# Kernel optimization log

Hardware: AMD Instinct MI355X
Metric: run time of the kernel (lower is better)

Reference implementation:

```python
import jax, jax.numpy as jnp
import numpy as np

NEG_SLOPE = 0.2

def setup_inputs() -> dict:
    key = jax.random.key(0)
    k1, k2, k3, k4 = jax.random.split(key, 4)
    B, n, d_in, d_out = 8, 2048, 128, 128
    x = jax.random.normal(k1, (B, n, d_in), dtype=jnp.float32)
    adj = jax.random.uniform(k2, (B, n, n), dtype=jnp.float32)
    # glorot init for W: std = sqrt(2/(fan_in+fan_out))
    W = jax.random.normal(k3, (d_in, d_out), dtype=jnp.float32) * np.sqrt(2.0 / (d_in + d_out))
    a = jax.random.normal(k4, (2 * d_out,), dtype=jnp.float32) * np.sqrt(2.0 / (2 * d_out + 1))
    return {"x": x, "adj": adj, "W": W, "a": a}

def reference(x, adj, W, a):
    d_out = W.shape[1]
    h = jnp.einsum('bni,io->bno', x, W)               # [B,n,d_out]
    x_weighted = jnp.einsum('bnm,bmo->bno', adj, h)   # adj @ Wx
    # additive attention: a @ concat(h_i, h_j) == h_i@a_src + h_j@a_dst
    a_src, a_dst = a[:d_out], a[d_out:]
    s_i = h @ a_src                                   # [B,n]
    s_j = h @ a_dst                                   # [B,n]
    e = jax.nn.leaky_relu(s_i[:, :, None] + s_j[:, None, :], NEG_SLOPE)  # [B,n,n]
    alpha = jax.nn.softmax(e, axis=2)
    out = jnp.einsum('bnm,bmo->bno', alpha, h) + x_weighted
    return jax.nn.leaky_relu(out, NEG_SLOPE)
```

## Files before the change

kernel.cpp:

```cpp
#include <hip/hip_runtime.h>
#include <hip/hip_bf16.h>

#define NEG 0.2f
#define LOG2E 1.4426950408889634f

typedef __attribute__((ext_vector_type(8))) short bf16x8;
typedef __attribute__((ext_vector_type(4))) float f32x4;
typedef __attribute__((ext_vector_type(16))) float f32x16;
typedef __attribute__((ext_vector_type(4))) int int4v;
typedef __attribute__((ext_vector_type(2))) int int2v;

__device__ __forceinline__ float lrelu(float t){ return fmaxf(t, NEG * t); }
__device__ __forceinline__ float fast_exp2(float x){
  float r; asm("v_exp_f32 %0, %1" : "=v"(r) : "v"(x)); return r;
}
__device__ __forceinline__ unsigned short f2bf(float f){
  union { float f; unsigned int u; } v; v.f = f;
  unsigned int r = v.u + 0x7FFFu + ((v.u >> 16) & 1u);
  return (unsigned short)(r >> 16);
}

__global__ __launch_bounds__(256) void k0_wt(const float* __restrict__ W,
                                             unsigned short* __restrict__ Wt){
  __shared__ __align__(16) unsigned short wl[128*136];
  const int t = threadIdx.x;
  {
    const int k = t >> 1, oh = (t & 1) * 64;
#pragma unroll 8
    for (int e = 0; e < 64; ++e)
      wl[(oh + e)*136 + k] = f2bf(W[k*128 + oh + e]);
  }
  __syncthreads();
  {
    const int o = t >> 1, ks = (t & 1) * 64;
#pragma unroll
    for (int g = 0; g < 8; ++g){
      int4v v = *(const int4v*)(wl + o*136 + ks + g*8);
      *(int4v*)(Wt + o*128 + ks + g*8) = v;
    }
  }
}

__global__ __launch_bounds__(256) void k1_fused(const float* __restrict__ x,
                                                const unsigned short* __restrict__ Wt,
                                                const float* __restrict__ a,
                                                unsigned short* __restrict__ ht,
                                                float* __restrict__ ssrcL,
                                                float* __restrict__ sdstL){
  __shared__ __align__(16) unsigned short wtl[128*136];
  __shared__ __align__(16) unsigned short xl[32*136];
  __shared__ __align__(16) unsigned short tlw[128*34];
  __shared__ float sred[2][4][2][16];
  const int t = threadIdx.x;
  const int bx = blockIdx.x;
  const int b  = bx >> 6;
  const int jt = bx & 63;
  const long rowbase = (long)bx * 32;
  {
    const int o = t >> 1, seg = (t & 1) * 64;
    const int4v* src = (const int4v*)(Wt + o*128 + seg);
    int4v* dst = (int4v*)(wtl + o*136 + seg);
#pragma unroll
    for (int g = 0; g < 8; ++g) dst[g] = src[g];
  }
  {
    const int i = t >> 3, ks = (t & 7) * 16;
    const f32x4* src = (const f32x4*)(x + (rowbase + i)*128 + ks);
    unsigned int q[8];
#pragma unroll
    for (int g = 0; g < 4; ++g){
      f32x4 v = src[g];
      q[g*2]   = (unsigned)f2bf(v[0]) | ((unsigned)f2bf(v[1]) << 16);
      q[g*2+1] = (unsigned)f2bf(v[2]) | ((unsigned)f2bf(v[3]) << 16);
    }
    int4v* dst = (int4v*)(xl + i*136 + ks);
    dst[0] = *(int4v*)&q[0];
    dst[1] = *(int4v*)&q[4];
  }
  __syncthreads();
  const int w = t >> 6, lane = t & 63, lr = lane & 15, hi = lane >> 4;
  f32x4 zro = {0.f, 0.f, 0.f, 0.f};
  f32x4 acc00 = zro, acc01 = zro, acc10 = zro, acc11 = zro;
#pragma unroll
  for (int ks = 0; ks < 4; ++ks){
    const bf16x8 a0 = *(const bf16x8*)(wtl + (w*32      + lr)*136 + ks*32 + hi*8);
    const bf16x8 a1 = *(const bf16x8*)(wtl + (w*32 + 16 + lr)*136 + ks*32 + hi*8);
    const bf16x8 b0 = *(const bf16x8*)(xl + (     lr)*136 + ks*32 + hi*8);
    const bf16x8 b1 = *(const bf16x8*)(xl + (16 + lr)*136 + ks*32 + hi*8);
    acc00 = __builtin_amdgcn_mfma_f32_16x16x32_bf16(a0, b0, acc00, 0, 0, 0);
    acc01 = __builtin_amdgcn_mfma_f32_16x16x32_bf16(a0, b1, acc01, 0, 0, 0);
    acc10 = __builtin_amdgcn_mfma_f32_16x16x32_bf16(a1, b0, acc10, 0, 0, 0);
    acc11 = __builtin_amdgcn_mfma_f32_16x16x32_bf16(a1, b1, acc11, 0, 0, 0);
  }
  {
    const f32x4 as0 = *(const f32x4*)(a +       w*32      + hi*4);
    const f32x4 as1 = *(const f32x4*)(a +       w*32 + 16 + hi*4);
    const f32x4 ad0 = *(const f32x4*)(a + 128 + w*32      + hi*4);
    const f32x4 ad1 = *(const f32x4*)(a + 128 + w*32 + 16 + hi*4);
    float ps0, ps1, pd0, pd1;
    {
      f32x4 u = acc00*as0 + acc10*as1;  ps0 = u[0]+u[1]+u[2]+u[3];
      f32x4 v = acc01*as0 + acc11*as1;  ps1 = v[0]+v[1]+v[2]+v[3];
      f32x4 p = acc00*ad0 + acc10*ad1;  pd0 = p[0]+p[1]+p[2]+p[3];
      f32x4 r = acc01*ad0 + acc11*ad1;  pd1 = r[0]+r[1]+r[2]+r[3];
    }
#pragma unroll
    for (int off = 16; off <= 32; off <<= 1){
      ps0 += __shfl_xor(ps0, off); ps1 += __shfl_xor(ps1, off);
      pd0 += __shfl_xor(pd0, off); pd1 += __shfl_xor(pd1, off);
    }
    if (hi == 0){
      sred[0][w][0][lr] = ps0; sred[0][w][1][lr] = ps1;
      sred[1][w][0][lr] = pd0; sred[1][w][1][lr] = pd1;
    }
  }
#pragma unroll
  for (int q = 0; q < 4; ++q){
    tlw[(w*32      + hi*4 + q)*34      + lr] = f2bf(acc00[q]);
    tlw[(w*32      + hi*4 + q)*34 + 16 + lr] = f2bf(acc01[q]);
    tlw[(w*32 + 16 + hi*4 + q)*34      + lr] = f2bf(acc10[q]);
    tlw[(w*32 + 16 + hi*4 + q)*34 + 16 + lr] = f2bf(acc11[q]);
  }
  __syncthreads();
  {
    const int o = t >> 1, jseg = (t & 1) * 16;
    const unsigned int* src = (const unsigned int*)(tlw + o*34 + jseg);
    unsigned int p[8];
#pragma unroll
    for (int g = 0; g < 8; ++g) p[g] = src[g];
    unsigned short* dst = ht + (long)b*262144 + (long)o*2048 + jt*32 + jseg;
    ((int4v*)dst)[0] = *(int4v*)&p[0];
    ((int4v*)dst)[1] = *(int4v*)&p[4];
  }
  if (t < 64){
    const int sel = t >> 5, jl = t & 31;
    const int ig = jl >> 4, l2 = jl & 15;
    const float s = sred[sel][0][ig][l2] + sred[sel][1][ig][l2]
                  + sred[sel][2][ig][l2] + sred[sel][3][ig][l2];
    if (sel == 0) ssrcL[rowbase + jl] = s * LOG2E;
    else          sdstL[rowbase + jl] = s * LOG2E;
  }
}

__global__ __launch_bounds__(256) void k2_max(const float* __restrict__ sdstL,
                                              float* __restrict__ M){
  __shared__ float red[4];
  const int b = blockIdx.x, t = threadIdx.x;
  const int lane = t & 63, w = t >> 6;
  const f32x4* sd = (const f32x4*)(sdstL + (long)b*2048 + t*8);
  f32x4 v0 = sd[0], v1 = sd[1];
  float mx = fmaxf(fmaxf(fmaxf(v0[0], v0[1]), fmaxf(v0[2], v0[3])),
                   fmaxf(fmaxf(v1[0], v1[1]), fmaxf(v1[2], v1[3])));
#pragma unroll
  for (int off = 1; off <= 32; off <<= 1) mx = fmaxf(mx, __shfl_xor(mx, off));
  if (lane == 0) red[w] = mx;
  __syncthreads();
  if (t == 0) M[b] = fmaxf(fmaxf(red[0], red[1]), fmaxf(red[2], red[3]));
}

__global__ __launch_bounds__(256) void k2_ml(const float* __restrict__ ssrcL,
                                             const float* __restrict__ sdstL,
                                             const float* __restrict__ M,
                                             float* __restrict__ carr){
  const int lane = threadIdx.x & 63;
  const long row = (long)blockIdx.x * 4 + (threadIdx.x >> 6);
  const int b = (int)(row >> 11);
  const float siL = ssrcL[row];
  const float mL = lrelu(siL + M[b]);
  const float* sd = sdstL + (long)b*2048;
  float sum = 0.f;
#pragma unroll
  for (int k = 0; k < 8; ++k){
    f32x4 v = *(const f32x4*)(sd + lane*4 + k*256);
#pragma unroll
    for (int e = 0; e < 4; ++e) sum += fast_exp2(lrelu(siL + v[e]) - mL);
  }
#pragma unroll
  for (int off = 1; off <= 32; off <<= 1) sum += __shfl_xor(sum, off);
  if (lane == 0) carr[row] = mL + __log2f(sum);
}

__global__ __launch_bounds__(512, 4) void k3_main(const float* __restrict__ adj,
                                                  const unsigned short* __restrict__ ht,
                                                  const float* __restrict__ ssrcL,
                                                  const float* __restrict__ sdstL,
                                                  const float* __restrict__ carr,
                                                  float* __restrict__ out){
  __shared__ __align__(16) char smem[40960];
  unsigned short (*httile)[2][128][32] = (unsigned short (*)[2][128][32])smem;
  unsigned short (*wtile)[32][64]      = (unsigned short (*)[32][64])(smem + 32768);
  float* red = (float*)smem;
  const int t    = threadIdx.x;
  const int bxr  = blockIdx.x;
  const int bx   = ((bxr & 7) << 6) | (bxr >> 3);
  const int b    = bx >> 6;
  const int i0   = (bx & 63) * 32;
  const int w    = t >> 6, lane = t & 63;
  const int cg   = w & 3, sh = w >> 2;
  const int r32  = lane & 31, hl = lane >> 5;
  const int r7   = r32 & 7;
  const long rowg = (long)b*2048 + i0 + r32;
  const float siL = ssrcL[rowg];
  const float Ci  = carr[rowg];
  const float* adjL = adj + rowg*2048 + w*8 + hl*4;
  const float* sdbL = sdstL + (long)b*2048 + w*8 + hl*4;
  const unsigned short* sgbase = ht + (long)b*262144
                               + (long)(cg*32 + (lane >> 2))*2048 + sh*32
                               + (((lane & 3) ^ ((lane >> 2) & 3))) * 8;

  f32x16 acc;
#pragma unroll
  for (int e = 0; e < 16; ++e) acc[e] = 0.f;
  f32x4 avA, dvA, avB, dvB;

#pragma unroll
  for (int rr = 0; rr < 2; ++rr)
    __builtin_amdgcn_global_load_lds(
      (const __attribute__((address_space(1))) void*)(sgbase + rr*32768),
      (__attribute__((address_space(3))) void*)&httile[0][sh][cg*32 + rr*16][0], 16, 0, 0);
  avA = *(const f32x4*)(adjL);      dvA = *(const f32x4*)(sdbL);
  avB = *(const f32x4*)(adjL + 64); dvB = *(const f32x4*)(sdbL + 64);

#define K3_STEP(KT, BUF, DO_STAGE, DO_REFILL, VMSTR, AV, DV) do{                 \
    if (DO_STAGE){                                                               \
      _Pragma("unroll")                                                          \
      for (int rr = 0; rr < 2; ++rr)                                             \
        __builtin_amdgcn_global_load_lds(                                        \
          (const __attribute__((address_space(1))) void*)(sgbase + ((KT)+1)*64 + rr*32768), \
          (__attribute__((address_space(3))) void*)&httile[(BUF)^1][sh][cg*32 + rr*16][0], 16, 0, 0); \
    }                                                                            \
    {  float wv[4];                                                              \
       _Pragma("unroll")                                                         \
       for (int e = 0; e < 4; ++e)                                               \
         wv[e] = AV[e] + fast_exp2(lrelu(siL + DV[e]) - Ci);                     \
       const unsigned p01 = __builtin_amdgcn_perm(__float_as_uint(wv[1]), __float_as_uint(wv[0]), 0x07060302u); \
       const unsigned p23 = __builtin_amdgcn_perm(__float_as_uint(wv[3]), __float_as_uint(wv[2]), 0x07060302u); \
       int2v iv = {(int)p01, (int)p23};                                          \
       *(int2v*)&wtile[BUF][r32][(w ^ r7)*8 + hl*4] = iv;                        \
    }                                                                            \
    if (DO_REFILL){                                                              \
      AV = *(const f32x4*)(adjL + ((KT)+2)*64);                                  \
      DV = *(const f32x4*)(sdbL + ((KT)+2)*64);                                  \
    }                                                                            \
    asm volatile("s_waitcnt vmcnt(" VMSTR ") lgkmcnt(0)" ::: "memory");          \
    __builtin_amdgcn_sched_barrier(0);                                           \
    __builtin_amdgcn_s_barrier();                                                \
    __builtin_amdgcn_sched_barrier(0);                                           \
    __builtin_amdgcn_s_setprio(1);                                               \
    _Pragma("unroll")                                                            \
    for (int g = 0; g < 2; ++g){                                                 \
      const bf16x8 afr = *(const bf16x8*)&wtile[BUF][r32][((sh*4 + g*2 + hl) ^ r7)*8]; \
      const bf16x8 bfr = *(const bf16x8*)&httile[BUF][sh][cg*32 + r32][((g*2 + hl) ^ (r32 & 3))*8]; \
      acc = __builtin_amdgcn_mfma_f32_32x32x16_bf16(afr, bfr, acc, 0, 0, 0);     \
    }                                                                            \
    __builtin_amdgcn_s_setprio(0);                                               \
    __builtin_amdgcn_sched_barrier(0);                                           \
  }while(0)

  for (int kt = 0; kt < 30; kt += 2){
    K3_STEP(kt,     0, 1, 1, "4", avA, dvA);
    K3_STEP(kt + 1, 1, 1, 1, "4", avB, dvB);
  }
  K3_STEP(30, 0, 1, 0, "4", avA, dvA);
  K3_STEP(31, 1, 0, 0, "0", avB, dvB);
#undef K3_STEP

  if (sh == 1){
#pragma unroll
    for (int rg = 0; rg < 16; ++rg){
      const int rr = (rg & 3) + 8*(rg >> 2) + 4*hl;
      red[cg*1024 + rr*32 + r32] = acc[rg];
    }
  }
  __syncthreads();
  if (sh == 0){
#pragma unroll
    for (int rg = 0; rg < 16; ++rg){
      const int rr = (rg & 3) + 8*(rg >> 2) + 4*hl;
      const float v = acc[rg] + red[cg*1024 + rr*32 + r32];
      out[((long)b*2048 + i0 + rr)*128 + cg*32 + r32] = lrelu(v);
    }
  }
}

extern "C" void kernel_launch(void* const* d_in, const int* in_sizes, int n_in,
                              void* d_out, int out_size, void* d_ws, size_t ws_size,
                              hipStream_t stream){
  const float* x   = (const float*)d_in[0];
  const float* adj = (const float*)d_in[1];
  const float* W   = (const float*)d_in[2];
  const float* a   = (const float*)d_in[3];
  float* out = (float*)d_out;
  char* ws = (char*)d_ws;

  unsigned short* ht    = (unsigned short*)(ws);
  float*          ssrcL = (float*)(ws + 4194304);
  float*          sdstL = (float*)(ws + 4259840);
  float*          carr  = (float*)(ws + 4325376);
  unsigned short* Wt    = (unsigned short*)(ws + 4390912);
  float*          M     = (float*)(ws + 4423680);

  k0_wt   <<<1,    256, 0, stream>>>(W, Wt);
  k1_fused<<<512,  256, 0, stream>>>(x, Wt, a, ht, ssrcL, sdstL);
  k2_max  <<<8,    256, 0, stream>>>(sdstL, M);
  k2_ml   <<<4096, 256, 0, stream>>>(ssrcL, sdstL, M, carr);
  k3_main <<<512,  512, 0, stream>>>(adj, ht, ssrcL, sdstL, carr, out);
}
```

Before: 61.05 us.

## Restructure main GAT kernel to 4 waves with 128-wide K tiles, drop split-K reduction

The main attention-aggregation kernel moves from 8 waves with a two-way split over K (and a shared-memory reduction at the end) to 4 waves. Each wave owns one 32-column output slice over the full K range, using K tiles of 128 instead of 64. This halves the number of barrier-separated steps and removes the final LDS reduction. Each thread now loads and converts 16 adj/score elements per step with wider vector stores, and the swizzle patterns change to match. In exchange the kernel uses double the LDS per block and fewer threads per block, which may cut occupancy and the latency hiding for the adj stream.

```diff
diff --git a/kernel.cpp b/kernel.cpp
--- a/kernel.cpp
+++ b/kernel.cpp
@@ -8,7 +8,6 @@
 typedef __attribute__((ext_vector_type(4))) float f32x4;
 typedef __attribute__((ext_vector_type(16))) float f32x16;
 typedef __attribute__((ext_vector_type(4))) int int4v;
-typedef __attribute__((ext_vector_type(2))) int int2v;
 
 __device__ __forceinline__ float lrelu(float t){ return fmaxf(t, NEG * t); }
 __device__ __forceinline__ float fast_exp2(float x){
@@ -180,106 +179,110 @@
   if (lane == 0) carr[row] = mL + __log2f(sum);
 }
 
-__global__ __launch_bounds__(512, 4) void k3_main(const float* __restrict__ adj,
+__global__ __launch_bounds__(256, 2) void k3_main(const float* __restrict__ adj,
                                                   const unsigned short* __restrict__ ht,
                                                   const float* __restrict__ ssrcL,
                                                   const float* __restrict__ sdstL,
                                                   const float* __restrict__ carr,
                                                   float* __restrict__ out){
-  __shared__ __align__(16) char smem[40960];
-  unsigned short (*httile)[2][128][32] = (unsigned short (*)[2][128][32])smem;
-  unsigned short (*wtile)[32][64]      = (unsigned short (*)[32][64])(smem + 32768);
-  float* red = (float*)smem;
+  __shared__ __align__(16) char smem[81920];
+  unsigned short (*httile)[128][128] = (unsigned short (*)[128][128])smem;
+  unsigned short (*wtile)[32][128]   = (unsigned short (*)[32][128])(smem + 65536);
   const int t    = threadIdx.x;
   const int bxr  = blockIdx.x;
   const int bx   = ((bxr & 7) << 6) | (bxr >> 3);
   const int b    = bx >> 6;
   const int i0   = (bx & 63) * 32;
   const int w    = t >> 6, lane = t & 63;
-  const int cg   = w & 3, sh = w >> 2;
   const int r32  = lane & 31, hl = lane >> 5;
-  const int r7   = r32 & 7;
+  const int xr   = r32 & 15;
+  const int c0   = w*4 + hl*2;
   const long rowg = (long)b*2048 + i0 + r32;
   const float siL = ssrcL[rowg];
   const float Ci  = carr[rowg];
-  const float* adjL = adj + rowg*2048 + w*8 + hl*4;
-  const float* sdbL = sdstL + (long)b*2048 + w*8 + hl*4;
-  const unsigned short* sgbase = ht + (long)b*262144
-                               + (long)(cg*32 + (lane >> 2))*2048 + sh*32
-                               + (((lane & 3) ^ ((lane >> 2) & 3))) * 8;
+  const float* adjL = adj + rowg*2048 + w*32 + hl*16;
+  const float* sdbL = sdstL + (long)b*2048 + w*32 + hl*16;
+  const unsigned short* sgrow = ht + (long)b*262144 + (long)(w*32 + (lane >> 4))*2048;
+  const int sch = (lane & 15) ^ (lane >> 4);
 
   f32x16 acc;
 #pragma unroll
   for (int e = 0; e < 16; ++e) acc[e] = 0.f;
-  f32x4 avA, dvA, avB, dvB;
-
-#pragma unroll
-  for (int rr = 0; rr < 2; ++rr)
-    __builtin_amdgcn_global_load_lds(
-      (const __attribute__((address_space(1))) void*)(sgbase + rr*32768),
-      (__attribute__((address_space(3))) void*)&httile[0][sh][cg*32 + rr*16][0], 16, 0, 0);
-  avA = *(const f32x4*)(adjL);      dvA = *(const f32x4*)(sdbL);
-  avB = *(const f32x4*)(adjL + 64); dvB = *(const f32x4*)(sdbL + 64);
+  f32x4 avA[4], dvA[4], avB[4], dvB[4];
+
+#define K3_STAGE(B2, WIN) do{                                                    \
+    _Pragma("unroll")                                                            \
+    for (int ii = 0; ii < 8; ++ii){                                              \
+      __builtin_amdgcn_global_load_lds(                                          \
+        (const __attribute__((address_space(1))) void*)                          \
+          (sgrow + (long)ii*8192 + (WIN) + (sch ^ ((ii*4) & 15))*8),             \
+        (__attribute__((address_space(3))) void*)&httile[B2][w*32 + ii*4][0],    \
+        16, 0, 0);                                                               \
+    }                                                                            \
+  }while(0)
+
+#define K3_REFILL(AV, DV, WIN) do{                                               \
+    _Pragma("unroll")                                                            \
+    for (int g = 0; g < 4; ++g){                                                 \
+      AV[g] = *(const f32x4*)(adjL + (WIN) + g*4);                               \
+      DV[g] = *(const f32x4*)(sdbL + (WIN) + g*4);                               \
+    }                                                                            \
+  }while(0)
+
+  K3_STAGE(0, 0);
+  K3_REFILL(avA, dvA, 0);
+  K3_REFILL(avB, dvB, 128);
+  asm volatile("s_waitcnt vmcnt(16)" ::: "memory");
+  __builtin_amdgcn_sched_barrier(0);
 
 #define K3_STEP(KT, BUF, DO_STAGE, DO_REFILL, VMSTR, AV, DV) do{                 \
-    if (DO_STAGE){                                                               \
-      _Pragma("unroll")                                                          \
-      for (int rr = 0; rr < 2; ++rr)                                             \
-        __builtin_amdgcn_global_load_lds(                                        \
-          (const __attribute__((address_space(1))) void*)(sgbase + ((KT)+1)*64 + rr*32768), \
-          (__attribute__((address_space(3))) void*)&httile[(BUF)^1][sh][cg*32 + rr*16][0], 16, 0, 0); \
+    if (DO_STAGE) K3_STAGE((BUF)^1, ((KT)+1)*128);                               \
+    {  unsigned pw[8];                                                           \
+       _Pragma("unroll")                                                         \
+       for (int g = 0; g < 4; ++g){                                              \
+         float w0 = AV[g][0] + fast_exp2(lrelu(siL + DV[g][0]) - Ci);            \
+         float w1 = AV[g][1] + fast_exp2(lrelu(siL + DV[g][1]) - Ci);            \
+         float w2 = AV[g][2] + fast_exp2(lrelu(siL + DV[g][2]) - Ci);            \
+         float w3 = AV[g][3] + fast_exp2(lrelu(siL + DV[g][3]) - Ci);            \
+         pw[g*2]   = __builtin_amdgcn_perm(__float_as_uint(w1), __float_as_uint(w0), 0x07060302u); \
+         pw[g*2+1] = __builtin_amdgcn_perm(__float_as_uint(w3), __float_as_uint(w2), 0x07060302u); \
+       }                                                                         \
+       int4v iv0 = {(int)pw[0], (int)pw[1], (int)pw[2], (int)pw[3]};             \
+       int4v iv1 = {(int)pw[4], (int)pw[5], (int)pw[6], (int)pw[7]};             \
+       *(int4v*)&wtile[BUF][r32][( c0      ^ xr)*8] = iv0;                       \
+       *(int4v*)&wtile[BUF][r32][((c0 + 1) ^ xr)*8] = iv1;                       \
     }                                                                            \
-    {  float wv[4];                                                              \
-       _Pragma("unroll")                                                         \
-       for (int e = 0; e < 4; ++e)                                               \
-         wv[e] = AV[e] + fast_exp2(lrelu(siL + DV[e]) - Ci);                     \
-       const unsigned p01 = __builtin_amdgcn_perm(__float_as_uint(wv[1]), __float_as_uint(wv[0]), 0x07060302u); \
-       const unsigned p23 = __builtin_amdgcn_perm(__float_as_uint(wv[3]), __float_as_uint(wv[2]), 0x07060302u); \
-       int2v iv = {(int)p01, (int)p23};                                          \
-       *(int2v*)&wtile[BUF][r32][(w ^ r7)*8 + hl*4] = iv;                        \
-    }                                                                            \
-    if (DO_REFILL){                                                              \
-      AV = *(const f32x4*)(adjL + ((KT)+2)*64);                                  \
-      DV = *(const f32x4*)(sdbL + ((KT)+2)*64);                                  \
-    }                                                                            \
+    if (DO_REFILL) K3_REFILL(AV, DV, ((KT)+2)*128);                              \
     asm volatile("s_waitcnt vmcnt(" VMSTR ") lgkmcnt(0)" ::: "memory");          \
     __builtin_amdgcn_sched_barrier(0);                                           \
     __builtin_amdgcn_s_barrier();                                                \
     __builtin_amdgcn_sched_barrier(0);                                           \
     __builtin_amdgcn_s_setprio(1);                                               \
     _Pragma("unroll")                                                            \
-    for (int g = 0; g < 2; ++g){                                                 \
-      const bf16x8 afr = *(const bf16x8*)&wtile[BUF][r32][((sh*4 + g*2 + hl) ^ r7)*8]; \
-      const bf16x8 bfr = *(const bf16x8*)&httile[BUF][sh][cg*32 + r32][((g*2 + hl) ^ (r32 & 3))*8]; \
+    for (int g = 0; g < 8; ++g){                                                 \
+      const int cp = ((g*2 + hl) ^ xr)*8;                                        \
+      const bf16x8 afr = *(const bf16x8*)&wtile[BUF][r32][cp];                   \
+      const bf16x8 bfr = *(const bf16x8*)&httile[BUF][w*32 + r32][cp];           \
       acc = __builtin_amdgcn_mfma_f32_32x32x16_bf16(afr, bfr, acc, 0, 0, 0);     \
     }                                                                            \
     __builtin_amdgcn_s_setprio(0);                                               \
     __builtin_amdgcn_sched_barrier(0);                                           \
   }while(0)
 
-  for (int kt = 0; kt < 30; kt += 2){
-    K3_STEP(kt,     0, 1, 1, "4", avA, dvA);
-    K3_STEP(kt + 1, 1, 1, 1, "4", avB, dvB);
-  }
-  K3_STEP(30, 0, 1, 0, "4", avA, dvA);
-  K3_STEP(31, 1, 0, 0, "0", avB, dvB);
+  for (int kt = 0; kt < 14; kt += 2){
+    K3_STEP(kt,     0, 1, 1, "16", avA, dvA);
+    K3_STEP(kt + 1, 1, 1, 1, "16", avB, dvB);
+  }
+  K3_STEP(14, 0, 1, 0, "16", avA, dvA);
+  K3_STEP(15, 1, 0, 0, "0",  avB, dvB);
 #undef K3_STEP
-
-  if (sh == 1){
-#pragma unroll
-    for (int rg = 0; rg < 16; ++rg){
-      const int rr = (rg & 3) + 8*(rg >> 2) + 4*hl;
-      red[cg*1024 + rr*32 + r32] = acc[rg];
-    }
-  }
-  __syncthreads();
-  if (sh == 0){
-#pragma unroll
-    for (int rg = 0; rg < 16; ++rg){
-      const int rr = (rg & 3) + 8*(rg >> 2) + 4*hl;
-      const float v = acc[rg] + red[cg*1024 + rr*32 + r32];
-      out[((long)b*2048 + i0 + rr)*128 + cg*32 + r32] = lrelu(v);
-    }
+#undef K3_STAGE
+#undef K3_REFILL
+
+#pragma unroll
+  for (int rg = 0; rg < 16; ++rg){
+    const int rr = (rg & 3) + 8*(rg >> 2) + 4*hl;
+    out[((long)b*2048 + i0 + rr)*128 + w*32 + r32] = lrelu(acc[rg]);
   }
 }
 
@@ -304,5 +307,5 @@
   k1_fused<<<512,  256, 0, stream>>>(x, Wt, a, ht, ssrcL, sdstL);
   k2_max  <<<8,    256, 0, stream>>>(sdstL, M);
   k2_ml   <<<4096, 256, 0, stream>>>(ssrcL, sdstL, M, carr);
-  k3_main <<<512,  512, 0, stream>>>(adj, ht, ssrcL, sdstL, carr, out);
-}
+  k3_main <<<512,  256, 0, stream>>>(adj, ht, ssrcL, sdstL, carr, out);
+}
```

New measurement: 56.59 us. -7.3%, faster.
